# Kernel tuning notes

Measured on AMD Instinct MI355X. Metric: run time of the kernel, lower is better.

The kernel has to match this reference:

```python
import jax, jax.numpy as jnp
import numpy as np

NUM_NODES = 50000
NUM_EDGES = 800000
NUM_FEATURES = 128
HIDDEN = 128
NUM_CLASSES = 40


def setup_inputs() -> dict:
    key = jax.random.key(0)
    ks = jax.random.split(key, 10)
    x = jax.random.normal(ks[0], (NUM_NODES, NUM_FEATURES), dtype=jnp.float32)
    edge_index = jax.random.randint(ks[1], (2, NUM_EDGES), 0, NUM_NODES, dtype=jnp.int32)
    def glorot(k, fan_in, fan_out):
        s = jnp.sqrt(6.0 / (fan_in + fan_out))
        return jax.random.uniform(k, (fan_in, fan_out), jnp.float32, -s, s)
    return {
        "x": x,
        "edge_index": edge_index,
        "W1": glorot(ks[2], NUM_FEATURES, HIDDEN), "b1": jnp.zeros((HIDDEN,), jnp.float32),
        "W2": glorot(ks[3], HIDDEN, HIDDEN),       "b2": jnp.zeros((HIDDEN,), jnp.float32),
        "W3": glorot(ks[4], HIDDEN, HIDDEN),       "b3": jnp.zeros((HIDDEN,), jnp.float32),
        "Wc": glorot(ks[5], HIDDEN, NUM_CLASSES),  "bc": jnp.zeros((NUM_CLASSES,), jnp.float32),
    }


def _gcn_norm(edge_index, num_nodes, dtype):
    # add self-loops, symmetric normalization D^{-1/2} (A+I) D^{-1/2}
    loops = jnp.arange(num_nodes, dtype=edge_index.dtype)
    src = jnp.concatenate([edge_index[0], loops])
    dst = jnp.concatenate([edge_index[1], loops])
    deg = jax.ops.segment_sum(jnp.ones_like(dst, dtype=dtype), dst, num_segments=num_nodes)
    dinv = jnp.where(deg > 0, jax.lax.rsqrt(deg), 0.0)
    norm = dinv[src] * dinv[dst]  # [E + N]
    return src, dst, norm


def _gcn_conv(h, W, b, src, dst, norm, num_nodes):
    h = h @ W                                  # [N, out]
    msg = h[src] * norm[:, None]               # gather + scale  [E+N, out]
    agg = jax.ops.segment_sum(msg, dst, num_segments=num_nodes)
    return agg + b


def reference(x, edge_index, W1, b1, W2, b2, W3, b3, Wc, bc):
    N = x.shape[0]
    src, dst, norm = _gcn_norm(edge_index, N, x.dtype)
    h = jax.nn.relu(_gcn_conv(x, W1, b1, src, dst, norm, N))
    h = jax.nn.relu(_gcn_conv(h, W2, b2, src, dst, norm, N))
    h = jax.nn.relu(_gcn_conv(h, W3, b3, src, dst, norm, N))
    out = h @ Wc + bc
    return (out, h)
```

## Files before the change

### kernel.cpp

```cpp
#include <hip/hip_runtime.h>

typedef float f32x4 __attribute__((ext_vector_type(4)));
typedef short s16x8 __attribute__((ext_vector_type(8)));

__device__ __forceinline__ float us2f(unsigned short u) {
    union { unsigned int i; float f; } v;
    v.i = ((unsigned int)u) << 16;
    return v.f;
}
__device__ __forceinline__ unsigned short f2us(float f) {
    union { unsigned int i; float f; } v; v.f = f;
    unsigned int r = v.i + 0x7fff + ((v.i >> 16) & 1);
    return (unsigned short)(r >> 16);
}

__global__ __launch_bounds__(256) void k_prep_hist(const float* __restrict__ W1,
                                                   const float* __restrict__ W2,
                                                   const float* __restrict__ W3,
                                                   const float* __restrict__ Wc,
                                                   unsigned short* __restrict__ img,
                                                   const int* __restrict__ dst, int E, int chunk,
                                                   int* __restrict__ bcnt, int* __restrict__ done,
                                                   int* __restrict__ bofs, int* __restrict__ gcur) {
    __shared__ int cnt[256];
    __shared__ int lastflag;
    int t = threadIdx.x;
    if (blockIdx.x < 256) {
        int r = (blockIdx.x << 1) | (t >> 7);
        int b = r >> 7, k = r & 127, n = t & 127;
        unsigned short *H, *L;
        float f;
        if (b < 3) {
            const float* W = (b == 0) ? W1 : ((b == 1) ? W2 : W3);
            H = img + b * 32768; L = H + 16384;
            f = W[k * 128 + n];
        } else {
            if (n >= 48) return;
            H = img + 3 * 32768; L = H + 6144;
            f = (n < 40) ? Wc[k * 40 + n] : 0.f;
        }
        unsigned short h = f2us(f);
        unsigned short l = f2us(f - us2f(h));
        int idx = n * 128 + ((((k >> 3) ^ (n & 15))) << 3) + (k & 7);
        H[idx] = h; L[idx] = l;
        return;
    }
    cnt[t] = 0; __syncthreads();
    int blk = blockIdx.x - 256;
    int s0 = blk * chunk;
    int s1 = s0 + chunk; if (s1 > E) s1 = E;
    for (int i = s0 + t; i < s1; i += 256) atomicAdd(&cnt[dst[i] >> 8], 1);
    __syncthreads();
    int c = cnt[t];
    if (c) atomicAdd(&bcnt[t], c);
    __syncthreads();
    if (t == 0) { __threadfence(); lastflag = (atomicAdd(done, 1) == 255); }
    __syncthreads();
    if (!lastflag) return;
    int v = __hip_atomic_load(&bcnt[t], __ATOMIC_RELAXED, __HIP_MEMORY_SCOPE_AGENT);
    cnt[t] = v; __syncthreads();
    for (int off = 1; off < 256; off <<= 1) {
        int x = (t >= off) ? cnt[t - off] : 0;
        __syncthreads();
        cnt[t] += x;
        __syncthreads();
    }
    int ex = cnt[t] - v;
    bofs[t] = ex; gcur[t] = ex;
    if (t == 255) bofs[256] = cnt[255];
}

template <bool ABF16>
__device__ __forceinline__ void gemm128_core(const void* __restrict__ Ap,
                                             const unsigned short* __restrict__ img,
                                             unsigned short* __restrict__ M, int N,
                                             int bid, int t,
                                             unsigned short* WsH, unsigned short* WsL) {
    {
        const uint4* s = (const uint4*)img;
        uint4* dH = (uint4*)WsH; uint4* dL = (uint4*)WsL;
#pragma unroll
        for (int i = 0; i < 8; i++) dH[t + i * 256] = s[t + i * 256];
#pragma unroll
        for (int i = 0; i < 8; i++) dL[t + i * 256] = s[2048 + t + i * 256];
    }
    __syncthreads();

    int w = t >> 6, lane = t & 63;
    int m = lane & 15, q = lane >> 4;
    int row0 = bid * 64 + w * 16;
    int gr = row0 + m;
    int grc = (gr < N) ? gr : (N - 1);
    const float* A32 = (const float*)Ap + (size_t)grc * 128;
    const unsigned short* A16 = (const unsigned short*)Ap + (size_t)grc * 128;
    int nbase = m * 128;

    f32x4 acc[8];
#pragma unroll
    for (int cb = 0; cb < 8; cb++) { acc[cb][0]=0.f; acc[cb][1]=0.f; acc[cb][2]=0.f; acc[cb][3]=0.f; }

#pragma unroll
    for (int ks = 0; ks < 4; ks++) {
        union { unsigned short u[8]; s16x8 v; } ah, al;
        if constexpr (ABF16) {
            ah.v = *(const s16x8*)&A16[ks * 32 + q * 8];
        } else {
            float4 f0 = ((const float4*)A32)[ks * 8 + q * 2];
            float4 f1 = ((const float4*)A32)[ks * 8 + q * 2 + 1];
            float fv[8] = {f0.x, f0.y, f0.z, f0.w, f1.x, f1.y, f1.z, f1.w};
#pragma unroll
            for (int j = 0; j < 8; j++) {
                unsigned short h = f2us(fv[j]);
                ah.u[j] = h;
                al.u[j] = f2us(fv[j] - us2f(h));
            }
        }
        int koff = (((ks * 4 + q) ^ m) & 15) << 3;
#pragma unroll
        for (int cb = 0; cb < 8; cb++) {
            int o = cb * 2048 + nbase + koff;
            s16x8 wh = *(const s16x8*)&WsH[o];
            s16x8 wl = *(const s16x8*)&WsL[o];
            acc[cb] = __builtin_amdgcn_mfma_f32_16x16x32_bf16(ah.v, wh, acc[cb], 0, 0, 0);
            acc[cb] = __builtin_amdgcn_mfma_f32_16x16x32_bf16(ah.v, wl, acc[cb], 0, 0, 0);
            if constexpr (!ABF16)
                acc[cb] = __builtin_amdgcn_mfma_f32_16x16x32_bf16(al.v, wh, acc[cb], 0, 0, 0);
        }
    }

#pragma unroll
    for (int r = 0; r < 4; r++) {
        int grow = row0 + q * 4 + r;
        if (grow < N) {
#pragma unroll
            for (int cb = 0; cb < 8; cb++)
                M[(size_t)grow * 128 + cb * 16 + m] = f2us(acc[cb][r]);
        }
    }
}

template <bool ABF16>
__global__ __launch_bounds__(256) void k_gemm128m(const void* __restrict__ Ap,
                                                  const unsigned short* __restrict__ img,
                                                  unsigned short* __restrict__ M, int N) {
    __shared__ __align__(16) unsigned short WsH[16384];
    __shared__ __align__(16) unsigned short WsL[16384];
    gemm128_core<ABF16>(Ap, img, M, N, blockIdx.x, threadIdx.x, WsH, WsL);
}

union KSM {
    struct { unsigned short H[16384]; unsigned short L[16384]; } w;
    int cnt[256];
};
__global__ __launch_bounds__(256) void k_sc1_gemm1(const int* __restrict__ src,
                                                   const int* __restrict__ dst, int E, int chunk,
                                                   int* __restrict__ gcur,
                                                   unsigned int* __restrict__ pk,
                                                   const float* __restrict__ x,
                                                   const unsigned short* __restrict__ img,
                                                   unsigned short* __restrict__ M, int N) {
    __shared__ __align__(16) KSM sm;
    int t = threadIdx.x;
    if (blockIdx.x < 256) {
        sm.cnt[t] = 0; __syncthreads();
        int s0 = blockIdx.x * chunk;
        int s1 = s0 + chunk; if (s1 > E) s1 = E;
        for (int i = s0 + t; i < s1; i += 256) atomicAdd(&sm.cnt[dst[i] >> 8], 1);
        __syncthreads();
        int base = atomicAdd(&gcur[t], sm.cnt[t]);
        sm.cnt[t] = base;
        __syncthreads();
        for (int i = s0 + t; i < s1; i += 256) {
            int d = dst[i];
            int slot = atomicAdd(&sm.cnt[d >> 8], 1);
            pk[slot] = ((unsigned int)src[i] << 8) | (unsigned int)(d & 255);
        }
        return;
    }
    gemm128_core<false>(x, img, M, N, blockIdx.x - 256, t, sm.w.H, sm.w.L);
}

__global__ __launch_bounds__(256) void k_csr_finish(const unsigned int* __restrict__ pk,
                                                    const int* __restrict__ bofs,
                                                    int* __restrict__ row_ptr,
                                                    int* __restrict__ bsum,
                                                    float* __restrict__ dinv,
                                                    int* __restrict__ csr,
                                                    int N, int E, int nb,
                                                    int* __restrict__ done2,
                                                    int* __restrict__ flag3) {
    __shared__ int cnt[256];
    __shared__ int s[256];
    __shared__ int lastflag;
    int t = threadIdx.x, b = blockIdx.x;
    cnt[t] = 0; __syncthreads();
    int s0 = bofs[b], s1 = bofs[b + 1];
    for (int i = s0 + t; i < s1; i += 256) atomicAdd(&cnt[pk[i] & 255], 1);
    __syncthreads();
    int v = cnt[t];
    s[t] = v; __syncthreads();
    for (int off = 1; off < 256; off <<= 1) {
        int x = (t >= off) ? s[t - off] : 0;
        __syncthreads();
        s[t] += x;
        __syncthreads();
    }
    int node = (b << 8) + t;
    int rp_local = s[t] - v;
    if (node < N) dinv[node] = rsqrtf((float)(v + 1));
    if (t == 255) __hip_atomic_store(&bsum[b], s[255], __ATOMIC_RELAXED, __HIP_MEMORY_SCOPE_AGENT);
    __syncthreads();
    if (t == 0) { __threadfence(); lastflag = (atomicAdd(done2, 1) == nb - 1); }
    __syncthreads();
    if (lastflag) {
        int vv = (t < nb) ? __hip_atomic_load(&bsum[t], __ATOMIC_RELAXED, __HIP_MEMORY_SCOPE_AGENT) : 0;
        s[t] = vv; __syncthreads();
        for (int off = 1; off < 256; off <<= 1) {
            int x = (t >= off) ? s[t - off] : 0;
            __syncthreads();
            s[t] += x;
            __syncthreads();
        }
        if (t < nb) __hip_atomic_store(&bsum[t], s[t] - vv, __ATOMIC_RELAXED, __HIP_MEMORY_SCOPE_AGENT);
        __syncthreads();
        if (t == 0) { __threadfence(); __hip_atomic_store(flag3, 1, __ATOMIC_RELEASE, __HIP_MEMORY_SCOPE_AGENT); }
    }
    if (t == 0) {
        while (__hip_atomic_load(flag3, __ATOMIC_ACQUIRE, __HIP_MEMORY_SCOPE_AGENT) == 0)
            __builtin_amdgcn_s_sleep(2);
    }
    __syncthreads();
    int base = __hip_atomic_load(&bsum[b], __ATOMIC_RELAXED, __HIP_MEMORY_SCOPE_AGENT);
    int rp = 0;
    if (node < N) { rp = rp_local + base; row_ptr[node] = rp; }
    cnt[t] = rp;
    __syncthreads();
    for (int i = s0 + t; i < s1; i += 256) {
        unsigned int vpk = pk[i];
        int slot = atomicAdd(&cnt[vpk & 255], 1);
        csr[slot] = (int)(vpk >> 8);
    }
    if (node == N - 1) row_ptr[N] = E;
}

template <bool OUT_BF16>
__global__ __launch_bounds__(256) void k_gather(const unsigned short* __restrict__ M,
                                                const int* __restrict__ csr,
                                                const int* __restrict__ row_ptr,
                                                const float* __restrict__ dinv,
                                                const float* __restrict__ bias,
                                                void* __restrict__ H, int N) {
    int w    = (blockIdx.x << 2) + (threadIdx.x >> 6);
    int lane = threadIdx.x & 63;
    if (w >= N) return;
    int g  = lane >> 4;
    int sl = lane & 15;

    const uint4* M16 = (const uint4*)M;
    float dv = dinv[w];
    float acc[8];
#pragma unroll
    for (int i = 0; i < 8; i++) acc[i] = 0.f;

    auto accum = [&](uint4 tv, float sc) {
        unsigned int uu[4] = {tv.x, tv.y, tv.z, tv.w};
#pragma unroll
        for (int i = 0; i < 4; i++) {
            acc[2 * i]     = fmaf(sc, us2f((unsigned short)(uu[i] & 0xffffu)), acc[2 * i]);
            acc[2 * i + 1] = fmaf(sc, us2f((unsigned short)(uu[i] >> 16)), acc[2 * i + 1]);
        }
    };

    if (g == 0) accum(M16[(size_t)w * 16 + sl], dv);

    int s0 = row_ptr[w], s1 = row_ptr[w + 1];
    for (int base = s0; base < s1; base += 64) {
        int n = s1 - base; if (n > 64) n = 64;
        int idx = (lane < n) ? csr[base + lane] : 0;
        int full = n >> 2;
        int rem  = n & 3;
        int j = 0;
        for (; j + 4 <= full; j += 4) {
            int u0 = __shfl(idx, (j + 0) * 4 + g);
            int u1 = __shfl(idx, (j + 1) * 4 + g);
            int u2 = __shfl(idx, (j + 2) * 4 + g);
            int u3 = __shfl(idx, (j + 3) * 4 + g);
            float d0 = dinv[u0], d1 = dinv[u1], d2 = dinv[u2], d3 = dinv[u3];
            uint4 t0 = M16[(size_t)u0 * 16 + sl];
            uint4 t1 = M16[(size_t)u1 * 16 + sl];
            uint4 t2 = M16[(size_t)u2 * 16 + sl];
            uint4 t3 = M16[(size_t)u3 * 16 + sl];
            accum(t0, d0); accum(t1, d1); accum(t2, d2); accum(t3, d3);
        }
        for (; j < full; j++) {
            int u = __shfl(idx, j * 4 + g);
            accum(M16[(size_t)u * 16 + sl], dinv[u]);
        }
        int ur = __shfl(idx, ((full << 2) + g) & 63);
        if (g < rem) accum(M16[(size_t)ur * 16 + sl], dinv[ur]);
    }

#pragma unroll
    for (int i = 0; i < 8; i++) {
        acc[i] += __shfl_xor(acc[i], 16);
        acc[i] += __shfl_xor(acc[i], 32);
    }

    const float4* b4 = (const float4*)bias;
    float4 b0 = b4[sl * 2], b1 = b4[sl * 2 + 1];
    float o[8];
    o[0] = fmaxf(fmaf(dv, acc[0], b0.x), 0.f);
    o[1] = fmaxf(fmaf(dv, acc[1], b0.y), 0.f);
    o[2] = fmaxf(fmaf(dv, acc[2], b0.z), 0.f);
    o[3] = fmaxf(fmaf(dv, acc[3], b0.w), 0.f);
    o[4] = fmaxf(fmaf(dv, acc[4], b1.x), 0.f);
    o[5] = fmaxf(fmaf(dv, acc[5], b1.y), 0.f);
    o[6] = fmaxf(fmaf(dv, acc[6], b1.z), 0.f);
    o[7] = fmaxf(fmaf(dv, acc[7], b1.w), 0.f);

    if (g == 0) {
        if constexpr (OUT_BF16) {
            uint4 p;
            p.x = (unsigned int)f2us(o[0]) | ((unsigned int)f2us(o[1]) << 16);
            p.y = (unsigned int)f2us(o[2]) | ((unsigned int)f2us(o[3]) << 16);
            p.z = (unsigned int)f2us(o[4]) | ((unsigned int)f2us(o[5]) << 16);
            p.w = (unsigned int)f2us(o[6]) | ((unsigned int)f2us(o[7]) << 16);
            ((uint4*)H)[(size_t)w * 16 + sl] = p;
        } else {
            float4* H4 = (float4*)H;
            H4[(size_t)w * 32 + sl * 2]     = make_float4(o[0], o[1], o[2], o[3]);
            H4[(size_t)w * 32 + sl * 2 + 1] = make_float4(o[4], o[5], o[6], o[7]);
        }
    }
}

__global__ __launch_bounds__(256) void k_gemm40m(const float* __restrict__ A,
                                                 const unsigned short* __restrict__ img,
                                                 const float* __restrict__ bc,
                                                 float* __restrict__ out, int N) {
    __shared__ __align__(16) unsigned short WsH[6144];
    __shared__ __align__(16) unsigned short WsL[6144];
    int t = threadIdx.x;
    {
        const uint4* s = (const uint4*)img;
        uint4* dH = (uint4*)WsH; uint4* dL = (uint4*)WsL;
#pragma unroll
        for (int i = 0; i < 3; i++) dH[t + i * 256] = s[t + i * 256];
#pragma unroll
        for (int i = 0; i < 3; i++) dL[t + i * 256] = s[768 + t + i * 256];
    }
    __syncthreads();

    int w = t >> 6, lane = t & 63;
    int m = lane & 15, q = lane >> 4;
    int row0 = blockIdx.x * 64 + w * 16;
    int gr = row0 + m;
    int grc = (gr < N) ? gr : (N - 1);
    const float4* Arow = (const float4*)(A + (size_t)grc * 128);
    int nbase = m * 128;

    f32x4 acc[3];
#pragma unroll
    for (int cb = 0; cb < 3; cb++) { acc[cb][0]=0.f; acc[cb][1]=0.f; acc[cb][2]=0.f; acc[cb][3]=0.f; }

#pragma unroll
    for (int ks = 0; ks < 4; ks++) {
        float4 f0 = Arow[ks * 8 + q * 2];
        float4 f1 = Arow[ks * 8 + q * 2 + 1];
        float fv[8] = {f0.x, f0.y, f0.z, f0.w, f1.x, f1.y, f1.z, f1.w};
        union { unsigned short u[8]; s16x8 v; } ah, al;
#pragma unroll
        for (int j = 0; j < 8; j++) {
            unsigned short h = f2us(fv[j]);
            ah.u[j] = h;
            al.u[j] = f2us(fv[j] - us2f(h));
        }
        int koff = (((ks * 4 + q) ^ m) & 15) << 3;
#pragma unroll
        for (int cb = 0; cb < 3; cb++) {
            int o = cb * 2048 + nbase + koff;
            s16x8 wh = *(const s16x8*)&WsH[o];
            s16x8 wl = *(const s16x8*)&WsL[o];
            acc[cb] = __builtin_amdgcn_mfma_f32_16x16x32_bf16(ah.v, wh, acc[cb], 0, 0, 0);
            acc[cb] = __builtin_amdgcn_mfma_f32_16x16x32_bf16(ah.v, wl, acc[cb], 0, 0, 0);
            acc[cb] = __builtin_amdgcn_mfma_f32_16x16x32_bf16(al.v, wh, acc[cb], 0, 0, 0);
        }
    }

#pragma unroll
    for (int r = 0; r < 4; r++) {
        int grow = row0 + q * 4 + r;
        if (grow < N) {
#pragma unroll
            for (int cb = 0; cb < 3; cb++) {
                int col = cb * 16 + m;
                if (col < 40) out[(size_t)grow * 40 + col] = acc[cb][r] + bc[col];
            }
        }
    }
}

extern "C" void kernel_launch(void* const* d_in, const int* in_sizes, int n_in,
                              void* d_out, int out_size, void* d_ws, size_t ws_size,
                              hipStream_t stream) {
    const float* x  = (const float*)d_in[0];
    const int*   ei = (const int*)d_in[1];
    const float* W1 = (const float*)d_in[2];
    const float* b1 = (const float*)d_in[3];
    const float* W2 = (const float*)d_in[4];
    const float* b2 = (const float*)d_in[5];
    const float* W3 = (const float*)d_in[6];
    const float* b3 = (const float*)d_in[7];
    const float* Wc = (const float*)d_in[8];
    const float* bc = (const float*)d_in[9];

    const int N = in_sizes[0] / 128;
    const int E = in_sizes[1] / 2;
    const int* src = ei;
    const int* dst = ei + E;

    char* ws = (char*)d_ws;
    size_t off = 0;
    auto alloc = [&](size_t bytes) -> void* {
        void* p = ws + off;
        off = (off + bytes + 255) & ~(size_t)255;
        return p;
    };
    unsigned short* Mbuf = (unsigned short*)alloc((size_t)N * 128 * 2);
    unsigned short* Hb   = (unsigned short*)alloc((size_t)N * 128 * 2);
    unsigned int* pk     = (unsigned int*)alloc((size_t)E * 4);
    unsigned short* img  = (unsigned short*)alloc((3 * 32768 + 2 * 6144) * 2);
    float* dinv    = (float*)alloc((size_t)N * 4);
    int*   row_ptr = (int*)alloc((size_t)(N + 1) * 4);
    int*   csr     = (int*)alloc((size_t)E * 4);
    int*   ctrl    = (int*)alloc(512 * 4);
    int*   bofs    = (int*)alloc(257 * 4);
    int*   gcur    = (int*)alloc(256 * 4);
    int*   bsum    = (int*)alloc(256 * 4);

    int* bcnt  = ctrl;
    int* done  = ctrl + 256;
    int* done2 = ctrl + 257;
    int* flag3 = ctrl + 258;

    float* out  = (float*)d_out;
    float* hbuf = out + (size_t)N * 40;

    const int nb  = (N + 255) / 256;
    const int chunk = (E + 255) / 256;

    const int gb  = (N + 63) / 64;
    const int gab = (N + 3) / 4;

    hipMemsetAsync(ctrl, 0, 512 * 4, stream);

    k_prep_hist<<<512, 256, 0, stream>>>(W1, W2, W3, Wc, img, dst, E, chunk,
                                         bcnt, done, bofs, gcur);
    k_sc1_gemm1<<<256 + gb, 256, 0, stream>>>(src, dst, E, chunk, gcur, pk,
                                              x, img, Mbuf, N);
    k_csr_finish<<<nb, 256, 0, stream>>>(pk, bofs, row_ptr, bsum, dinv, csr,
                                         N, E, nb, done2, flag3);

    k_gather<true><<<gab, 256, 0, stream>>>(Mbuf, csr, row_ptr, dinv, b1, Hb, N);
    k_gemm128m<true><<<gb, 256, 0, stream>>>(Hb, img + 32768, Mbuf, N);
    k_gather<true><<<gab, 256, 0, stream>>>(Mbuf, csr, row_ptr, dinv, b2, Hb, N);
    k_gemm128m<true><<<gb, 256, 0, stream>>>(Hb, img + 2 * 32768, Mbuf, N);
    k_gather<false><<<gab, 256, 0, stream>>>(Mbuf, csr, row_ptr, dinv, b3, hbuf, N);
    k_gemm40m<<<gb, 256, 0, stream>>>(hbuf, img + 3 * 32768, bc, out, N);
}
```

Before: 288.1 us.

## Prescale GEMM outputs by source dinv and split gather into column passes

```diff
diff --git a/kernel.cpp b/kernel.cpp
--- a/kernel.cpp
+++ b/kernel.cpp
@@ -2,6 +2,7 @@
 
 typedef float f32x4 __attribute__((ext_vector_type(4)));
 typedef short s16x8 __attribute__((ext_vector_type(8)));
+typedef unsigned int u32x2 __attribute__((ext_vector_type(2)));
 
 __device__ __forceinline__ float us2f(unsigned short u) {
     union { unsigned int i; float f; } v;
@@ -21,7 +22,8 @@
                                                    unsigned short* __restrict__ img,
                                                    const int* __restrict__ dst, int E, int chunk,
                                                    int* __restrict__ bcnt, int* __restrict__ done,
-                                                   int* __restrict__ bofs, int* __restrict__ gcur) {
+                                                   int* __restrict__ bofs, int* __restrict__ gcur,
+                                                   int* __restrict__ deg) {
     __shared__ int cnt[256];
     __shared__ int lastflag;
     int t = threadIdx.x;
@@ -49,7 +51,11 @@
     int blk = blockIdx.x - 256;
     int s0 = blk * chunk;
     int s1 = s0 + chunk; if (s1 > E) s1 = E;
-    for (int i = s0 + t; i < s1; i += 256) atomicAdd(&cnt[dst[i] >> 8], 1);
+    for (int i = s0 + t; i < s1; i += 256) {
+        int d = dst[i];
+        atomicAdd(&cnt[d >> 8], 1);
+        atomicAdd(&deg[d], 1);
+    }
     __syncthreads();
     int c = cnt[t];
     if (c) atomicAdd(&bcnt[t], c);
@@ -70,9 +76,11 @@
     if (t == 255) bofs[256] = cnt[255];
 }
 
-template <bool ABF16>
+template <bool ABF16, bool MAKE_DINV>
 __device__ __forceinline__ void gemm128_core(const void* __restrict__ Ap,
                                              const unsigned short* __restrict__ img,
+                                             const int* __restrict__ deg,
+                                             float* __restrict__ dinv,
                                              unsigned short* __restrict__ M, int N,
                                              int bid, int t,
                                              unsigned short* WsH, unsigned short* WsL) {
@@ -132,9 +140,16 @@
     for (int r = 0; r < 4; r++) {
         int grow = row0 + q * 4 + r;
         if (grow < N) {
+            float dv;
+            if constexpr (MAKE_DINV) {
+                dv = rsqrtf((float)deg[grow] + 1.0f);
+                if (m == 0) dinv[grow] = dv;
+            } else {
+                dv = dinv[grow];
+            }
 #pragma unroll
             for (int cb = 0; cb < 8; cb++)
-                M[(size_t)grow * 128 + cb * 16 + m] = f2us(acc[cb][r]);
+                M[(size_t)grow * 128 + cb * 16 + m] = f2us(acc[cb][r] * dv);
         }
     }
 }
@@ -142,10 +157,12 @@
 template <bool ABF16>
 __global__ __launch_bounds__(256) void k_gemm128m(const void* __restrict__ Ap,
                                                   const unsigned short* __restrict__ img,
+                                                  const float* __restrict__ dinv,
                                                   unsigned short* __restrict__ M, int N) {
     __shared__ __align__(16) unsigned short WsH[16384];
     __shared__ __align__(16) unsigned short WsL[16384];
-    gemm128_core<ABF16>(Ap, img, M, N, blockIdx.x, threadIdx.x, WsH, WsL);
+    gemm128_core<ABF16, false>(Ap, img, nullptr, (float*)dinv, M, N,
+                               blockIdx.x, threadIdx.x, WsH, WsL);
 }
 
 union KSM {
@@ -158,6 +175,8 @@
                                                    unsigned int* __restrict__ pk,
                                                    const float* __restrict__ x,
                                                    const unsigned short* __restrict__ img,
+                                                   const int* __restrict__ deg,
+                                                   float* __restrict__ dinv,
                                                    unsigned short* __restrict__ M, int N) {
     __shared__ __align__(16) KSM sm;
     int t = threadIdx.x;
@@ -177,14 +196,13 @@
         }
         return;
     }
-    gemm128_core<false>(x, img, M, N, blockIdx.x - 256, t, sm.w.H, sm.w.L);
+    gemm128_core<false, true>(x, img, deg, dinv, M, N, blockIdx.x - 256, t, sm.w.H, sm.w.L);
 }
 
 __global__ __launch_bounds__(256) void k_csr_finish(const unsigned int* __restrict__ pk,
                                                     const int* __restrict__ bofs,
                                                     int* __restrict__ row_ptr,
                                                     int* __restrict__ bsum,
-                                                    float* __restrict__ dinv,
                                                     int* __restrict__ csr,
                                                     int N, int E, int nb,
                                                     int* __restrict__ done2,
@@ -207,7 +225,6 @@
     }
     int node = (b << 8) + t;
     int rp_local = s[t] - v;
-    if (node < N) dinv[node] = rsqrtf((float)(v + 1));
     if (t == 255) __hip_atomic_store(&bsum[b], s[255], __ATOMIC_RELAXED, __HIP_MEMORY_SCOPE_AGENT);
     __syncthreads();
     if (t == 0) { __threadfence(); lastflag = (atomicAdd(done2, 1) == nb - 1); }
@@ -244,92 +261,65 @@
 }
 
 template <bool OUT_BF16>
-__global__ __launch_bounds__(256) void k_gather(const unsigned short* __restrict__ M,
-                                                const int* __restrict__ csr,
-                                                const int* __restrict__ row_ptr,
-                                                const float* __restrict__ dinv,
-                                                const float* __restrict__ bias,
-                                                void* __restrict__ H, int N) {
-    int w    = (blockIdx.x << 2) + (threadIdx.x >> 6);
+__global__ __launch_bounds__(256) void k_gather_p(const unsigned short* __restrict__ M,
+                                                  const int* __restrict__ csr,
+                                                  const int* __restrict__ row_ptr,
+                                                  const float* __restrict__ dinv,
+                                                  const float* __restrict__ bias,
+                                                  void* __restrict__ H, int N) {
+    int w = (blockIdx.x << 2) + (threadIdx.x >> 6);
+    if (w >= N) return;
+    int pass = blockIdx.y;
     int lane = threadIdx.x & 63;
-    if (w >= N) return;
-    int g  = lane >> 4;
-    int sl = lane & 15;
-
-    const uint4* M16 = (const uint4*)M;
-    float dv = dinv[w];
-    float acc[8];
-#pragma unroll
-    for (int i = 0; i < 8; i++) acc[i] = 0.f;
-
-    auto accum = [&](uint4 tv, float sc) {
-        unsigned int uu[4] = {tv.x, tv.y, tv.z, tv.w};
-#pragma unroll
-        for (int i = 0; i < 4; i++) {
-            acc[2 * i]     = fmaf(sc, us2f((unsigned short)(uu[i] & 0xffffu)), acc[2 * i]);
-            acc[2 * i + 1] = fmaf(sc, us2f((unsigned short)(uu[i] >> 16)), acc[2 * i + 1]);
-        }
+    int sub  = lane & 7;
+    int slot = lane >> 3;
+
+    const u32x2* M2 = (const u32x2*)M;
+    int poff = pass * 8 + sub;
+
+    float acc[4] = {0.f, 0.f, 0.f, 0.f};
+    auto accum = [&](u32x2 v) {
+        acc[0] += us2f((unsigned short)(v[0] & 0xffffu));
+        acc[1] += us2f((unsigned short)(v[0] >> 16));
+        acc[2] += us2f((unsigned short)(v[1] & 0xffffu));
+        acc[3] += us2f((unsigned short)(v[1] >> 16));
     };
 
-    if (g == 0) accum(M16[(size_t)w * 16 + sl], dv);
+    if (slot == 0) accum(M2[(size_t)w * 32 + poff]);
 
     int s0 = row_ptr[w], s1 = row_ptr[w + 1];
-    for (int base = s0; base < s1; base += 64) {
-        int n = s1 - base; if (n > 64) n = 64;
-        int idx = (lane < n) ? csr[base + lane] : 0;
-        int full = n >> 2;
-        int rem  = n & 3;
-        int j = 0;
-        for (; j + 4 <= full; j += 4) {
-            int u0 = __shfl(idx, (j + 0) * 4 + g);
-            int u1 = __shfl(idx, (j + 1) * 4 + g);
-            int u2 = __shfl(idx, (j + 2) * 4 + g);
-            int u3 = __shfl(idx, (j + 3) * 4 + g);
-            float d0 = dinv[u0], d1 = dinv[u1], d2 = dinv[u2], d3 = dinv[u3];
-            uint4 t0 = M16[(size_t)u0 * 16 + sl];
-            uint4 t1 = M16[(size_t)u1 * 16 + sl];
-            uint4 t2 = M16[(size_t)u2 * 16 + sl];
-            uint4 t3 = M16[(size_t)u3 * 16 + sl];
-            accum(t0, d0); accum(t1, d1); accum(t2, d2); accum(t3, d3);
-        }
-        for (; j < full; j++) {
-            int u = __shfl(idx, j * 4 + g);
-            accum(M16[(size_t)u * 16 + sl], dinv[u]);
-        }
-        int ur = __shfl(idx, ((full << 2) + g) & 63);
-        if (g < rem) accum(M16[(size_t)ur * 16 + sl], dinv[ur]);
-    }
-
-#pragma unroll
-    for (int i = 0; i < 8; i++) {
+    for (int base = s0; base < s1; base += 8) {
+        int i = base + slot;
+        int ic = (i < s1) ? i : (s1 - 1);
+        int u = __builtin_nontemporal_load(&csr[ic]);
+        u32x2 mv = M2[(size_t)u * 32 + poff];
+        if (i >= s1) { mv[0] = 0u; mv[1] = 0u; }
+        accum(mv);
+    }
+
+#pragma unroll
+    for (int i = 0; i < 4; i++) {
+        acc[i] += __shfl_xor(acc[i], 8);
         acc[i] += __shfl_xor(acc[i], 16);
         acc[i] += __shfl_xor(acc[i], 32);
     }
 
-    const float4* b4 = (const float4*)bias;
-    float4 b0 = b4[sl * 2], b1 = b4[sl * 2 + 1];
-    float o[8];
-    o[0] = fmaxf(fmaf(dv, acc[0], b0.x), 0.f);
-    o[1] = fmaxf(fmaf(dv, acc[1], b0.y), 0.f);
-    o[2] = fmaxf(fmaf(dv, acc[2], b0.z), 0.f);
-    o[3] = fmaxf(fmaf(dv, acc[3], b0.w), 0.f);
-    o[4] = fmaxf(fmaf(dv, acc[4], b1.x), 0.f);
-    o[5] = fmaxf(fmaf(dv, acc[5], b1.y), 0.f);
-    o[6] = fmaxf(fmaf(dv, acc[6], b1.z), 0.f);
-    o[7] = fmaxf(fmaf(dv, acc[7], b1.w), 0.f);
-
-    if (g == 0) {
+    float dv = dinv[w];
+    float4 bv = ((const float4*)bias)[pass * 8 + sub];
+    float o0 = fmaxf(fmaf(dv, acc[0], bv.x), 0.f);
+    float o1 = fmaxf(fmaf(dv, acc[1], bv.y), 0.f);
+    float o2 = fmaxf(fmaf(dv, acc[2], bv.z), 0.f);
+    float o3 = fmaxf(fmaf(dv, acc[3], bv.w), 0.f);
+
+    if (slot == 0) {
         if constexpr (OUT_BF16) {
-            uint4 p;
-            p.x = (unsigned int)f2us(o[0]) | ((unsigned int)f2us(o[1]) << 16);
-            p.y = (unsigned int)f2us(o[2]) | ((unsigned int)f2us(o[3]) << 16);
-            p.z = (unsigned int)f2us(o[4]) | ((unsigned int)f2us(o[5]) << 16);
-            p.w = (unsigned int)f2us(o[6]) | ((unsigned int)f2us(o[7]) << 16);
-            ((uint4*)H)[(size_t)w * 16 + sl] = p;
+            u32x2 p;
+            p[0] = (unsigned int)f2us(o0) | ((unsigned int)f2us(o1) << 16);
+            p[1] = (unsigned int)f2us(o2) | ((unsigned int)f2us(o3) << 16);
+            __builtin_nontemporal_store(p, &((u32x2*)H)[(size_t)w * 32 + poff]);
         } else {
-            float4* H4 = (float4*)H;
-            H4[(size_t)w * 32 + sl * 2]     = make_float4(o[0], o[1], o[2], o[3]);
-            H4[(size_t)w * 32 + sl * 2 + 1] = make_float4(o[4], o[5], o[6], o[7]);
+            f32x4 p = {o0, o1, o2, o3};
+            __builtin_nontemporal_store(p, &((f32x4*)H)[(size_t)w * 32 + pass * 8 + sub]);
         }
     }
 }
@@ -433,7 +423,7 @@
     float* dinv    = (float*)alloc((size_t)N * 4);
     int*   row_ptr = (int*)alloc((size_t)(N + 1) * 4);
     int*   csr     = (int*)alloc((size_t)E * 4);
-    int*   ctrl    = (int*)alloc(512 * 4);
+    int*   ctrl    = (int*)alloc((size_t)(512 + N) * 4);
     int*   bofs    = (int*)alloc(257 * 4);
     int*   gcur    = (int*)alloc(256 * 4);
     int*   bsum    = (int*)alloc(256 * 4);
@@ -442,6 +432,7 @@
     int* done  = ctrl + 256;
     int* done2 = ctrl + 257;
     int* flag3 = ctrl + 258;
+    int* deg   = ctrl + 512;
 
     float* out  = (float*)d_out;
     float* hbuf = out + (size_t)N * 40;
@@ -451,20 +442,21 @@
 
     const int gb  = (N + 63) / 64;
     const int gab = (N + 3) / 4;
-
-    hipMemsetAsync(ctrl, 0, 512 * 4, stream);
+    dim3 ggrid(gab, 4);
+
+    (void)hipMemsetAsync(ctrl, 0, (size_t)(512 + N) * 4, stream);
 
     k_prep_hist<<<512, 256, 0, stream>>>(W1, W2, W3, Wc, img, dst, E, chunk,
-                                         bcnt, done, bofs, gcur);
+                                         bcnt, done, bofs, gcur, deg);
     k_sc1_gemm1<<<256 + gb, 256, 0, stream>>>(src, dst, E, chunk, gcur, pk,
-                                              x, img, Mbuf, N);
-    k_csr_finish<<<nb, 256, 0, stream>>>(pk, bofs, row_ptr, bsum, dinv, csr,
+                                              x, img, deg, dinv, Mbuf, N);
+    k_csr_finish<<<nb, 256, 0, stream>>>(pk, bofs, row_ptr, bsum, csr,
                                          N, E, nb, done2, flag3);
 
-    k_gather<true><<<gab, 256, 0, stream>>>(Mbuf, csr, row_ptr, dinv, b1, Hb, N);
-    k_gemm128m<true><<<gb, 256, 0, stream>>>(Hb, img + 32768, Mbuf, N);
-    k_gather<true><<<gab, 256, 0, stream>>>(Mbuf, csr, row_ptr, dinv, b2, Hb, N);
-    k_gemm128m<true><<<gb, 256, 0, stream>>>(Hb, img + 2 * 32768, Mbuf, N);
-    k_gather<false><<<gab, 256, 0, stream>>>(Mbuf, csr, row_ptr, dinv, b3, hbuf, N);
+    k_gather_p<true><<<ggrid, 256, 0, stream>>>(Mbuf, csr, row_ptr, dinv, b1, Hb, N);
+    k_gemm128m<true><<<gb, 256, 0, stream>>>(Hb, img + 32768, dinv, Mbuf, N);
+    k_gather_p<true><<<ggrid, 256, 0, stream>>>(Mbuf, csr, row_ptr, dinv, b2, Hb, N);
+    k_gemm128m<true><<<gb, 256, 0, stream>>>(Hb, img + 2 * 32768, dinv, Mbuf, N);
+    k_gather_p<false><<<ggrid, 256, 0, stream>>>(Mbuf, csr, row_ptr, dinv, b3, hbuf, N);
     k_gemm40m<<<gb, 256, 0, stream>>>(hbuf, img + 3 * 32768, bc, out, N);
 }
```

Measured after the change: 523.2 us. 1.82x slower.
